# Kernel optimization log

Hardware: AMD Instinct MI355X
Metric: run time of the kernel (lower is better)

Reference implementation:

```python
import jax, jax.numpy as jnp
import numpy as np

N_NODES = 20000
N_EDGES = 40000
H = 64          # n_hidden
F_ATOM = 62     # n_atom_features (< H, triggers zero-pad path)
F_BOND = 6      # n_bond_features
B = 512         # number of graphs in batch
T = 2           # message passing steps


def setup_inputs() -> dict:
    key = jax.random.key(0)
    ks = jax.random.split(key, 20)
    s = 0.05  # small init scale to avoid selu/tanh saturation
    inp = {
        'node_features': jax.random.normal(ks[0], (N_NODES, F_ATOM), jnp.float32),
        'edge_features': jax.random.normal(ks[1], (N_EDGES, F_BOND), jnp.float32),
        'edge_domain': jax.random.randint(ks[2], (N_EDGES,), 0, N_NODES, jnp.int32),
        'edge_range': jax.random.randint(ks[3], (N_EDGES,), 0, N_NODES, jnp.int32),
        'graph_id': jnp.sort(jax.random.randint(ks[4], (N_NODES,), 0, B, jnp.int32)),
        # EdgeNetwork params (weights stored [in, out], i.e. torch W.T)
        'Wm': jax.random.normal(ks[5], (F_BOND, H), jnp.float32) * s,
        'bm': jnp.zeros((H,), jnp.float32),
        'Ew': jax.random.normal(ks[6], (H, H * H), jnp.float32) * s,  # E.weight used as mm(mlp, E.weight): [H, H*H]
        # update2 linears (T=2)
        'Wu0': jax.random.normal(ks[7], (H, H), jnp.float32) * s,
        'bu0': jnp.zeros((H,), jnp.float32),
        'Wu1': jax.random.normal(ks[8], (H, H), jnp.float32) * s,
        'bu1': jnp.zeros((H,), jnp.float32),
        # atom_embed
        'Wae': jax.random.normal(ks[9], (H, H), jnp.float32) * s,
        'bae': jnp.zeros((H,), jnp.float32),
        # AggregateReadout.R
        'WR': jax.random.normal(ks[10], (H, H), jnp.float32) * s,
        'bR': jnp.zeros((H,), jnp.float32),
        # mlp + out head
        'Wmlp': jax.random.normal(ks[11], (H, H), jnp.float32) * s,
        'bmlp': jnp.zeros((H,), jnp.float32),
        'Wout': jax.random.normal(ks[12], (H, 1), jnp.float32) * s,
        'bout': jnp.zeros((1,), jnp.float32),
    }
    return inp


def reference(node_features, edge_features, edge_domain, edge_range, graph_id,
              Wm, bm, Ew, Wu0, bu0, Wu1, bu1, Wae, bae, WR, bR,
              Wmlp, bmlp, Wout, bout):
    # pad node features up to n_hidden (original zero-pads when narrower)
    h = jnp.pad(node_features, ((0, 0), (0, H - F_ATOM)))  # [N, H]

    # EdgeNetwork: edge-conditioned per-edge HxH weight matrix.
    # Edge features are constant across T, so A is identical each step;
    # compute once (original recomputes the same values every iteration).
    mlp_features = jax.nn.relu(edge_features @ Wm + bm)      # [E, H]
    A = (mlp_features @ Ew).reshape(-1, H, H)                # [E, H, H]

    for Wu, bu in ((Wu0, bu0), (Wu1, bu1)):
        hj = h[edge_range]                                   # gather [E, H]
        edge_message = jnp.einsum('eij,ej->ei', A, hj)       # bmm [E, H]
        message = jax.ops.segment_sum(edge_message, edge_domain,
                                      num_segments=N_NODES)  # scatter-add [N, H]
        h = jax.nn.selu(message @ Wu + bu + h)

    atom_embedding = h @ Wae + bae                           # [N, H]
    # AggregateReadout
    atom_activation = jax.nn.selu(atom_embedding @ WR + bR)  # [N, H]
    graph_sum = jax.ops.segment_sum(atom_activation, graph_id, num_segments=B)
    graph_embedding = jnp.tanh(graph_sum)                    # [B, H]

    mlp_out = jax.nn.relu(graph_embedding @ Wmlp + bmlp)     # [B, H]
    out = mlp_out @ Wout + bout                              # [B, 1]
    return out.reshape(-1, 1)
```

## Files before the change

### kernel.cpp

```cpp
#include <hip/hip_runtime.h>
#include <math.h>

#define NN 20000
#define NE 40000
#define H 64
#define F_ATOM 62
#define F_BOND 6
#define NB 512

typedef _Float16 f16x8 __attribute__((ext_vector_type(8)));
typedef float f32x16 __attribute__((ext_vector_type(16)));

__device__ __forceinline__ float selu_f(float x) {
    const float scale = 1.0507009873554805f;
    const float alpha = 1.6732632423543772f;
    return scale * (x > 0.0f ? x : alpha * (__expf(x) - 1.0f));
}

__device__ __forceinline__ f16x8 splat8h(_Float16 x) {
    union { _Float16 h[2]; unsigned u; } p;
    p.h[0] = x; p.h[1] = x;
    union { unsigned u[4]; f16x8 v; } r;
    r.u[0] = p.u; r.u[1] = p.u; r.u[2] = p.u; r.u[3] = p.u;
    return r.v;
}

__global__ void prep_kernel(const float* __restrict__ nf, const float* __restrict__ ef,
                            const float* __restrict__ Wm, const float* __restrict__ bm,
                            const float* __restrict__ Ew,
                            float* __restrict__ h, _Float16* __restrict__ h_h,
                            unsigned* __restrict__ mlp2, _Float16* __restrict__ ewb,
                            float* __restrict__ msg, float* __restrict__ gsum) {
    const int bid = blockIdx.x;
    const int t = threadIdx.x;
    if (bid < 625) {
        __shared__ float st[64][65];
        const int el = t & 63;
        const int ig = t >> 6;
        const int e = bid * 64 + el;
        const float* efe = ef + e * F_BOND;
        const float e0 = efe[0], e1 = efe[1], e2 = efe[2];
        const float e3 = efe[3], e4 = efe[4], e5 = efe[5];
#pragma unroll
        for (int p = 0; p < 16; ++p) {
            const int i = ig * 16 + p;
            float s = bm[i];
            s = fmaf(e0, Wm[0 * H + i], s);
            s = fmaf(e1, Wm[1 * H + i], s);
            s = fmaf(e2, Wm[2 * H + i], s);
            s = fmaf(e3, Wm[3 * H + i], s);
            s = fmaf(e4, Wm[4 * H + i], s);
            s = fmaf(e5, Wm[5 * H + i], s);
            st[i][el] = fmaxf(s, 0.0f);
        }
        __syncthreads();
        const int p = t >> 3;
        const int ch = t & 7;
#pragma unroll
        for (int j = 0; j < 8; ++j) {
            const int e_l = ch * 8 + j;
            union { unsigned u; _Float16 hh[2]; } pk;
            pk.hh[0] = (_Float16)st[2 * p][e_l];
            pk.hh[1] = (_Float16)st[2 * p + 1][e_l];
            mlp2[(size_t)p * NE + bid * 64 + e_l] = pk.u;
        }
    } else if (bid < 5625) {
        int idx = (bid - 625) * 256 + t;
        int n = idx >> 6, c = idx & 63;
        float v = (c < F_ATOM) ? nf[n * F_ATOM + c] : 0.0f;
        h[idx] = v;
        h_h[idx] = (_Float16)v;
    } else if (bid < 5753) {
        int tid = (bid - 5625) * 256 + t;
        int l = tid & 63;
        int nt = (tid >> 6) & 1;
        int c = tid >> 7;
        int kk = c >> 2;
        int jbase = (c & 3) * 16 + (l >> 5) * 8;
        int i = nt * 32 + (l & 31);
        const float* src = Ew + kk * 4096 + i * 64 + jbase;
        _Float16* dst = ewb + tid * 8;
#pragma unroll
        for (int u = 0; u < 8; ++u) dst[u] = (_Float16)src[u];
    } else if (bid < 7003) {
        int idx = (bid - 5753) * 256 + t;
        reinterpret_cast<float4*>(msg)[idx] = make_float4(0.f, 0.f, 0.f, 0.f);
    } else {
        int idx = (bid - 7003) * 256 + t;
        reinterpret_cast<float4*>(gsum)[idx] = make_float4(0.f, 0.f, 0.f, 0.f);
    }
}

__global__ __launch_bounds__(128, 2) void edge_message_mfma(
    const _Float16* __restrict__ h_h, const unsigned* __restrict__ mlp2,
    const int* __restrict__ ed, const int* __restrict__ er,
    const _Float16* __restrict__ ewb, float* __restrict__ msg)
{
    __shared__ char sm[49152];
    __shared__ int edom_s[64];

    const int t = threadIdx.x;
    const int lane = t & 63;
    const int kg = t >> 6;
    const int l31 = lane & 31;
    const int hf = lane >> 5;
    const int eb = blockIdx.x * 64;

    if (t < 64) edom_s[t] = ed[eb + t];

    const int eA = eb + l31;
    const int eB = eA + 32;
    const int gA = er[eA], gB = er[eB];

    f16x8 hjA[4], hjB[4];
#pragma unroll
    for (int cq = 0; cq < 4; ++cq) {
        hjA[cq] = *reinterpret_cast<const f16x8*>(h_h + gA * 64 + cq * 16 + hf * 8);
        hjB[cq] = *reinterpret_cast<const f16x8*>(h_h + gB * 64 + cq * 16 + hf * 8);
    }

    unsigned mvA[16], mvB[16];
#pragma unroll
    for (int pp = 0; pp < 16; ++pp) {
        mvA[pp] = mlp2[(size_t)(kg * 16 + pp) * NE + eA];
        mvB[pp] = mlp2[(size_t)(kg * 16 + pp) * NE + eB];
    }

    asm volatile("s_waitcnt vmcnt(0)" ::: "memory");

    char* wbase = sm + kg * 24576;
    auto stage = [&](int s) {
        const char* gs = reinterpret_cast<const char*>(ewb) +
                         ((size_t)(kg * 32 + s) << 13) + lane * 16;
        char* lb = wbase + (s % 3) * 8192 + lane * 16;
#pragma unroll
        for (int r = 0; r < 8; ++r) {
            __builtin_amdgcn_global_load_lds(
                (const __attribute__((address_space(1))) void*)(gs + r * 1024),
                (__attribute__((address_space(3))) void*)(lb + r * 1024),
                16, 0, 0);
        }
    };

    f32x16 a00, a01, a10, a11;
#pragma unroll
    for (int i = 0; i < 16; ++i) { a00[i] = 0.f; a01[i] = 0.f; a10[i] = 0.f; a11[i] = 0.f; }

    stage(0);
    stage(1);

#pragma unroll
    for (int s = 0; s < 32; ++s) {
        if (s < 31) asm volatile("s_waitcnt vmcnt(8)" ::: "memory");
        else        asm volatile("s_waitcnt vmcnt(0)" ::: "memory");
        if (s < 30) stage(s + 2);
        const char* buf = wbase + (s % 3) * 8192;
        union { unsigned u; _Float16 hh[2]; } ua, ub;
        ua.u = mvA[s >> 1]; ub.u = mvB[s >> 1];
        f16x8 sA = splat8h(ua.hh[s & 1]);
        f16x8 sB = splat8h(ub.hh[s & 1]);
#pragma unroll
        for (int cq = 0; cq < 4; ++cq) {
            f16x8 b0 = *reinterpret_cast<const f16x8*>(buf + (cq * 2 + 0) * 1024 + lane * 16);
            f16x8 b1 = *reinterpret_cast<const f16x8*>(buf + (cq * 2 + 1) * 1024 + lane * 16);
            f16x8 aA = sA * hjA[cq];
            f16x8 aB = sB * hjB[cq];
            a00 = __builtin_amdgcn_mfma_f32_32x32x16_f16(aA, b0, a00, 0, 0, 0);
            a01 = __builtin_amdgcn_mfma_f32_32x32x16_f16(aA, b1, a01, 0, 0, 0);
            a10 = __builtin_amdgcn_mfma_f32_32x32x16_f16(aB, b0, a10, 0, 0, 0);
            a11 = __builtin_amdgcn_mfma_f32_32x32x16_f16(aB, b1, a11, 0, 0, 0);
        }
    }

    float* X = reinterpret_cast<float*>(sm);
    __syncthreads();
    if (kg == 1) {
#pragma unroll
        for (int r = 0; r < 16; ++r) {
            const int m = (r & 3) + 8 * (r >> 2) + 4 * hf;
            X[m * 64 + l31]             = a00[r];
            X[m * 64 + 32 + l31]        = a01[r];
            X[(32 + m) * 64 + l31]      = a10[r];
            X[(32 + m) * 64 + 32 + l31] = a11[r];
        }
    }
    __syncthreads();
    if (kg == 0) {
#pragma unroll
        for (int r = 0; r < 16; ++r) {
            const int m = (r & 3) + 8 * (r >> 2) + 4 * hf;
            const int domA = edom_s[m];
            const int domB = edom_s[32 + m];
            atomicAdd(&msg[domA * 64 + l31],      a00[r] + X[m * 64 + l31]);
            atomicAdd(&msg[domA * 64 + 32 + l31], a01[r] + X[m * 64 + 32 + l31]);
            atomicAdd(&msg[domB * 64 + l31],      a10[r] + X[(32 + m) * 64 + l31]);
            atomicAdd(&msg[domB * 64 + 32 + l31], a11[r] + X[(32 + m) * 64 + 32 + l31]);
        }
    }
}

__global__ void node_update_kernel(float* __restrict__ msg, const float* __restrict__ Wu,
                                   const float* __restrict__ bu, float* __restrict__ h,
                                   _Float16* __restrict__ h_h) {
    __shared__ float ms[4][68];
    int t = threadIdx.x;
    int nb = blockIdx.x * 4;
    int ln = t >> 6, i = t & 63;
    int o = (nb + ln) * H + i;
    ms[ln][i] = msg[o];
    msg[o] = 0.0f;
    __syncthreads();
    float s = bu[i];
#pragma unroll
    for (int k = 0; k < H; ++k) s = fmaf(ms[ln][k], Wu[k * H + i], s);
    float v = selu_f(s + h[o]);
    h[o] = v;
    h_h[o] = (_Float16)v;
}

__global__ void embed_readout_kernel(const float* __restrict__ h, const float* __restrict__ Wae,
                                     const float* __restrict__ bae, const float* __restrict__ WR,
                                     const float* __restrict__ bR, const int* __restrict__ gid,
                                     float* __restrict__ gsum) {
    __shared__ float hs[4][68];
    __shared__ float as_[4][68];
    int t = threadIdx.x;
    int nb = blockIdx.x * 4;
    int ln = t >> 6, i = t & 63;
    hs[ln][i] = h[(nb + ln) * H + i];
    __syncthreads();
    float s = bae[i];
#pragma unroll
    for (int k = 0; k < H; ++k) s = fmaf(hs[ln][k], Wae[k * H + i], s);
    as_[ln][i] = s;
    __syncthreads();
    float s2 = bR[i];
#pragma unroll
    for (int k = 0; k < H; ++k) s2 = fmaf(as_[ln][k], WR[k * H + i], s2);
    atomicAdd(&gsum[gid[nb + ln] * H + i], selu_f(s2));
}

__global__ void final_kernel(const float* __restrict__ gsum, const float* __restrict__ Wmlp,
                             const float* __restrict__ bmlp, const float* __restrict__ Wout,
                             const float* __restrict__ bout, float* __restrict__ out) {
    __shared__ float ge[64];
    int g = blockIdx.x, i = threadIdx.x;
    ge[i] = tanhf(gsum[g * H + i]);
    __syncthreads();
    float s = bmlp[i];
#pragma unroll
    for (int k = 0; k < H; ++k) s = fmaf(ge[k], Wmlp[k * H + i], s);
    float mo = fmaxf(s, 0.0f) * Wout[i];
#pragma unroll
    for (int off = 32; off > 0; off >>= 1) mo += __shfl_down(mo, off);
    if (i == 0) out[g] = mo + bout[0];
}

extern "C" void kernel_launch(void* const* d_in, const int* in_sizes, int n_in,
                              void* d_out, int out_size, void* d_ws, size_t ws_size,
                              hipStream_t stream) {
    const float* nf   = (const float*)d_in[0];
    const float* ef   = (const float*)d_in[1];
    const int*   ed   = (const int*)d_in[2];
    const int*   er   = (const int*)d_in[3];
    const int*   gid  = (const int*)d_in[4];
    const float* Wm   = (const float*)d_in[5];
    const float* bm   = (const float*)d_in[6];
    const float* Ew   = (const float*)d_in[7];
    const float* Wu0  = (const float*)d_in[8];
    const float* bu0  = (const float*)d_in[9];
    const float* Wu1  = (const float*)d_in[10];
    const float* bu1  = (const float*)d_in[11];
    const float* Wae  = (const float*)d_in[12];
    const float* bae  = (const float*)d_in[13];
    const float* WR   = (const float*)d_in[14];
    const float* bR   = (const float*)d_in[15];
    const float* Wmlp = (const float*)d_in[16];
    const float* bmlp = (const float*)d_in[17];
    const float* Wout = (const float*)d_in[18];
    const float* bout = (const float*)d_in[19];
    float* out = (float*)d_out;

    float* ws = (float*)d_ws;
    float*    h    = ws;
    float*    msg  = ws + 1280000;
    float*    gsum = ws + 2560000;
    unsigned* mlp2 = (unsigned*)(ws + 2592768);
    _Float16* h_h  = (_Float16*)(ws + 3872768);
    _Float16* ewb  = (_Float16*)(ws + 4512768);

    prep_kernel<<<7035, 256, 0, stream>>>(nf, ef, Wm, bm, Ew, h, h_h, mlp2, ewb, msg, gsum);

    for (int stepi = 0; stepi < 2; ++stepi) {
        edge_message_mfma<<<625, 128, 0, stream>>>(h_h, mlp2, ed, er, ewb, msg);
        node_update_kernel<<<NN / 4, 256, 0, stream>>>(msg, stepi ? Wu1 : Wu0,
                                                       stepi ? bu1 : bu0, h, h_h);
    }

    embed_readout_kernel<<<NN / 4, 256, 0, stream>>>(h, Wae, bae, WR, bR, gid, gsum);
    final_kernel<<<NB, 64, 0, stream>>>(gsum, Wmlp, bmlp, Wout, bout, out);
}
```

Before: 128.6 us.

## Drop fp32 h buffer, fuse second node update with embed/readout, add MFMA setprio

Removes the fp32 copy of the node state and keeps only the fp16 h_h. The residual is now read back from fp16, which adds rounding error across steps. The second node update is fused into the embed/readout kernel, cutting one launch and one round trip of h through global memory. s_setprio is also raised around the MFMA inner loop of the edge kernel to favour the matrix-issuing wave.

After: 127.9 us, median of 2. Within noise of the previous version (-0.5%).

```diff
diff --git a/kernel.cpp b/kernel.cpp
--- a/kernel.cpp
+++ b/kernel.cpp
@@ -28,7 +28,7 @@
 __global__ void prep_kernel(const float* __restrict__ nf, const float* __restrict__ ef,
                             const float* __restrict__ Wm, const float* __restrict__ bm,
                             const float* __restrict__ Ew,
-                            float* __restrict__ h, _Float16* __restrict__ h_h,
+                            _Float16* __restrict__ h_h,
                             unsigned* __restrict__ mlp2, _Float16* __restrict__ ewb,
                             float* __restrict__ msg, float* __restrict__ gsum) {
     const int bid = blockIdx.x;
@@ -67,9 +67,7 @@
     } else if (bid < 5625) {
         int idx = (bid - 625) * 256 + t;
         int n = idx >> 6, c = idx & 63;
-        float v = (c < F_ATOM) ? nf[n * F_ATOM + c] : 0.0f;
-        h[idx] = v;
-        h_h[idx] = (_Float16)v;
+        h_h[idx] = (_Float16)((c < F_ATOM) ? nf[n * F_ATOM + c] : 0.0f);
     } else if (bid < 5753) {
         int tid = (bid - 5625) * 256 + t;
         int l = tid & 63;
@@ -159,6 +157,7 @@
         ua.u = mvA[s >> 1]; ub.u = mvB[s >> 1];
         f16x8 sA = splat8h(ua.hh[s & 1]);
         f16x8 sB = splat8h(ub.hh[s & 1]);
+        __builtin_amdgcn_s_setprio(1);
 #pragma unroll
         for (int cq = 0; cq < 4; ++cq) {
             f16x8 b0 = *reinterpret_cast<const f16x8*>(buf + (cq * 2 + 0) * 1024 + lane * 16);
@@ -170,6 +169,7 @@
             a10 = __builtin_amdgcn_mfma_f32_32x32x16_f16(aB, b0, a10, 0, 0, 0);
             a11 = __builtin_amdgcn_mfma_f32_32x32x16_f16(aB, b1, a11, 0, 0, 0);
         }
+        __builtin_amdgcn_s_setprio(0);
     }
 
     float* X = reinterpret_cast<float*>(sm);
@@ -200,8 +200,7 @@
 }
 
 __global__ void node_update_kernel(float* __restrict__ msg, const float* __restrict__ Wu,
-                                   const float* __restrict__ bu, float* __restrict__ h,
-                                   _Float16* __restrict__ h_h) {
+                                   const float* __restrict__ bu, _Float16* __restrict__ h_h) {
     __shared__ float ms[4][68];
     int t = threadIdx.x;
     int nb = blockIdx.x * 4;
@@ -213,31 +212,37 @@
     float s = bu[i];
 #pragma unroll
     for (int k = 0; k < H; ++k) s = fmaf(ms[ln][k], Wu[k * H + i], s);
-    float v = selu_f(s + h[o]);
-    h[o] = v;
-    h_h[o] = (_Float16)v;
-}
-
-__global__ void embed_readout_kernel(const float* __restrict__ h, const float* __restrict__ Wae,
-                                     const float* __restrict__ bae, const float* __restrict__ WR,
-                                     const float* __restrict__ bR, const int* __restrict__ gid,
-                                     float* __restrict__ gsum) {
-    __shared__ float hs[4][68];
-    __shared__ float as_[4][68];
+    h_h[o] = (_Float16)selu_f(s + (float)h_h[o]);
+}
+
+__global__ void upd2_embed_readout(const float* __restrict__ msg, const float* __restrict__ Wu,
+                                   const float* __restrict__ bu, const _Float16* __restrict__ h_h,
+                                   const float* __restrict__ Wae, const float* __restrict__ bae,
+                                   const float* __restrict__ WR, const float* __restrict__ bR,
+                                   const int* __restrict__ gid, float* __restrict__ gsum) {
+    __shared__ float ms[4][68];
+    __shared__ float hn[4][68];
+    __shared__ float ae[4][68];
     int t = threadIdx.x;
     int nb = blockIdx.x * 4;
     int ln = t >> 6, i = t & 63;
-    hs[ln][i] = h[(nb + ln) * H + i];
-    __syncthreads();
-    float s = bae[i];
-#pragma unroll
-    for (int k = 0; k < H; ++k) s = fmaf(hs[ln][k], Wae[k * H + i], s);
-    as_[ln][i] = s;
-    __syncthreads();
-    float s2 = bR[i];
-#pragma unroll
-    for (int k = 0; k < H; ++k) s2 = fmaf(as_[ln][k], WR[k * H + i], s2);
-    atomicAdd(&gsum[gid[nb + ln] * H + i], selu_f(s2));
+    int o = (nb + ln) * H + i;
+    ms[ln][i] = msg[o];
+    __syncthreads();
+    float s = bu[i];
+#pragma unroll
+    for (int k = 0; k < H; ++k) s = fmaf(ms[ln][k], Wu[k * H + i], s);
+    hn[ln][i] = selu_f(s + (float)h_h[o]);
+    __syncthreads();
+    float s2 = bae[i];
+#pragma unroll
+    for (int k = 0; k < H; ++k) s2 = fmaf(hn[ln][k], Wae[k * H + i], s2);
+    ae[ln][i] = s2;
+    __syncthreads();
+    float s3 = bR[i];
+#pragma unroll
+    for (int k = 0; k < H; ++k) s3 = fmaf(ae[ln][k], WR[k * H + i], s3);
+    atomicAdd(&gsum[gid[nb + ln] * H + i], selu_f(s3));
 }
 
 __global__ void final_kernel(const float* __restrict__ gsum, const float* __restrict__ Wmlp,
@@ -282,21 +287,19 @@
     float* out = (float*)d_out;
 
     float* ws = (float*)d_ws;
-    float*    h    = ws;
     float*    msg  = ws + 1280000;
     float*    gsum = ws + 2560000;
     unsigned* mlp2 = (unsigned*)(ws + 2592768);
     _Float16* h_h  = (_Float16*)(ws + 3872768);
     _Float16* ewb  = (_Float16*)(ws + 4512768);
 
-    prep_kernel<<<7035, 256, 0, stream>>>(nf, ef, Wm, bm, Ew, h, h_h, mlp2, ewb, msg, gsum);
-
-    for (int stepi = 0; stepi < 2; ++stepi) {
-        edge_message_mfma<<<625, 128, 0, stream>>>(h_h, mlp2, ed, er, ewb, msg);
-        node_update_kernel<<<NN / 4, 256, 0, stream>>>(msg, stepi ? Wu1 : Wu0,
-                                                       stepi ? bu1 : bu0, h, h_h);
-    }
-
-    embed_readout_kernel<<<NN / 4, 256, 0, stream>>>(h, Wae, bae, WR, bR, gid, gsum);
+    prep_kernel<<<7035, 256, 0, stream>>>(nf, ef, Wm, bm, Ew, h_h, mlp2, ewb, msg, gsum);
+
+    edge_message_mfma<<<625, 128, 0, stream>>>(h_h, mlp2, ed, er, ewb, msg);
+    node_update_kernel<<<NN / 4, 256, 0, stream>>>(msg, Wu0, bu0, h_h);
+    edge_message_mfma<<<625, 128, 0, stream>>>(h_h, mlp2, ed, er, ewb, msg);
+    upd2_embed_readout<<<NN / 4, 256, 0, stream>>>(msg, Wu1, bu1, h_h,
+                                                   Wae, bae, WR, bR, gid, gsum);
+
     final_kernel<<<NB, 64, 0, stream>>>(gsum, Wmlp, bmlp, Wout, bout, out);
 }
```
